# Optimization experiments

Measured on AMD Instinct MI355X. Metric: run time of the kernel, lower is better.

The kernel has to match this reference:

```python
import jax, jax.numpy as jnp
import numpy as np

IN_F = 1024
OUT_F = 1024
GRID_SIZE = 5
SPLINE_ORDER = 3
GRID_RANGE = (-1.0, 1.0)


def _make_grid():
    h = (GRID_RANGE[1] - GRID_RANGE[0]) / GRID_SIZE
    g = jnp.arange(-SPLINE_ORDER, GRID_SIZE + SPLINE_ORDER + 1, dtype=jnp.float32) * h + GRID_RANGE[0]
    return jnp.broadcast_to(g, (IN_F, g.shape[0]))  # (F, grid_size + 2*order + 1)


def setup_inputs() -> dict:
    key = jax.random.key(0)
    k1, k2, k3, k4 = jax.random.split(key, 4)
    B = 8192
    x = jax.random.normal(k1, (B, IN_F), dtype=jnp.float32)
    base_weight = jax.random.normal(k2, (OUT_F, IN_F), dtype=jnp.float32) / np.sqrt(IN_F)
    # mimic reset_parameters: uniform noise scaled by scale_noise/grid_size
    spline_weight = (jax.random.uniform(k3, (OUT_F, IN_F, GRID_SIZE + SPLINE_ORDER)) - 0.5) * (0.1 / GRID_SIZE)
    spline_scaler = jax.random.normal(k4, (OUT_F, IN_F), dtype=jnp.float32) / np.sqrt(IN_F)
    grid = _make_grid()
    return {"x": x, "base_weight": base_weight, "spline_weight": spline_weight,
            "spline_scaler": spline_scaler, "grid": grid}


def b_splines(x, grid):
    # x: (B, F); grid: (F, G) with G = grid_size + 2*order + 1
    xe = x[:, :, None]  # (B, F, 1)
    bases = ((xe >= grid[:, :-1]) & (xe < grid[:, 1:])).astype(x.dtype)  # (B, F, G-1)
    for k in range(1, SPLINE_ORDER + 1):
        left = (xe - grid[:, : -(k + 1)]) / (grid[:, k:-1] - grid[:, : -(k + 1)])
        right = (grid[:, k + 1 :] - xe) / (grid[:, k + 1 :] - grid[:, 1:-k])
        bases = left * bases[:, :, :-1] + right * bases[:, :, 1:]
    return bases  # (B, F, grid_size + order)


def reference(x, base_weight, spline_weight, spline_scaler, grid):
    base_out = jax.nn.silu(x) @ base_weight.T  # (B, O)
    basis = b_splines(x, grid)  # (B, F, C)
    scaled_w = spline_weight * spline_scaler[:, :, None]  # (O, F, C)
    spline_out = jnp.einsum('bfc,ofc->bo', basis, scaled_w)
    return base_out + spline_out
```

## Files before the change

### kernel.cpp

```cpp
#include <hip/hip_runtime.h>
#include <hip/hip_bf16.h>

#define IN_F   1024
#define OUT_F  1024
#define NCH    9
#define KDIM   (IN_F * NCH)
#define BATCH  8192

#define BM 256
#define BN 128
#define BK 64
#define NT (KDIM / BK)
#define ABUF_OFF (BM * BK)
#define BUFSZ (BM * BK + BN * BK)

typedef __attribute__((ext_vector_type(4))) float  f32x4;
typedef __attribute__((ext_vector_type(8))) __bf16 bf16x8;

typedef __attribute__((address_space(3))) unsigned short       lds_u16;
typedef const __attribute__((address_space(1))) unsigned short glb_u16;

__device__ inline unsigned short f2bf(float f) {
    union { float f; unsigned int u; } v; v.f = f;
    unsigned int u = v.u;
    unsigned int r = (u + 0x7FFFu + ((u >> 16) & 1u)) >> 16;
    return (unsigned short)r;
}

__global__ void wgt_kernel(const float* __restrict__ bw,
                           const float* __restrict__ sw,
                           const float* __restrict__ sc,
                           unsigned short* __restrict__ W) {
    int idx = blockIdx.x * blockDim.x + threadIdx.x;
    if (idx >= OUT_F * IN_F) return;
    float scale = sc[idx];
    const float4* swp = (const float4*)(sw + (size_t)idx * 8);
    float4 w0 = swp[0], w1 = swp[1];
    int o = idx >> 10, f = idx & 1023;
    size_t base = (size_t)o * KDIM + (size_t)f * NCH;
    W[base + 0] = f2bf(w0.x * scale);
    W[base + 1] = f2bf(w0.y * scale);
    W[base + 2] = f2bf(w0.z * scale);
    W[base + 3] = f2bf(w0.w * scale);
    W[base + 4] = f2bf(w1.x * scale);
    W[base + 5] = f2bf(w1.y * scale);
    W[base + 6] = f2bf(w1.z * scale);
    W[base + 7] = f2bf(w1.w * scale);
    W[base + 8] = f2bf(bw[idx]);
}

__global__ void act_kernel(const float* __restrict__ x,
                           unsigned short* __restrict__ A,
                           int row0, int nrows) {
    int idx = blockIdx.x * blockDim.x + threadIdx.x;
    if (idx >= nrows * IN_F) return;
    int r = idx >> 10;
    int f = idx & 1023;
    float xv = x[(size_t)(row0 + r) * IN_F + f];

    float s = xv / (1.0f + __expf(-xv));

    float t  = (xv + 2.2f) * 2.5f;
    float jf = floorf(t);
    int   j  = (int)jf;
    float u  = t - jf;
    float u2 = u * u, u3 = u2 * u;
    float p0 = u3 * (1.0f / 6.0f);
    float p1 = (-3.0f * u3 + 3.0f * u2 + 3.0f * u + 1.0f) * (1.0f / 6.0f);
    float p2 = (3.0f * u3 - 6.0f * u2 + 4.0f) * (1.0f / 6.0f);
    float om = 1.0f - u;
    float p3 = om * om * om * (1.0f / 6.0f);
    bool valid = (xv >= -2.2f) && (xv < 2.2f);

    unsigned short outv[NCH];
#pragma unroll
    for (int c = 0; c < 8; ++c) {
        int p = j - c;
        float v = 0.0f;
        if (valid)
            v = (p == 0) ? p0 : (p == 1) ? p1 : (p == 2) ? p2 : (p == 3) ? p3 : 0.0f;
        outv[c] = f2bf(v);
    }
    outv[8] = f2bf(s);

    size_t base = (size_t)r * KDIM + (size_t)f * NCH;
#pragma unroll
    for (int c = 0; c < NCH; ++c) A[base + c] = outv[c];
}


#define DECLA(i) \
    const int ciA##i = (i) * 512 + tid; \
    const unsigned short* srcA##i = A + (size_t)(m0 + (ciA##i >> 3)) * KDIM \
        + ((((ciA##i) & 7) ^ ((ciA##i >> 3) & 7)) << 3); \
    const int ldsA##i = (ciA##i) << 3;

#define DECLB(i) \
    const int ciB##i = (i) * 512 + tid; \
    const unsigned short* srcB##i = W + (size_t)(n0 + (ciB##i >> 3)) * KDIM \
        + ((((ciB##i) & 7) ^ ((ciB##i >> 3) & 7)) << 3); \
    const int ldsB##i = ABUF_OFF + ((ciB##i) << 3);

#define STAGE_A(i) do { \
    __builtin_amdgcn_global_load_lds((glb_u16*)srcA##i, (lds_u16*)nb + ldsA##i, 16, 0, 0); \
    srcA##i += BK; } while (0)

#define STAGE_B(i) do { \
    __builtin_amdgcn_global_load_lds((glb_u16*)srcB##i, (lds_u16*)nb + ldsB##i, 16, 0, 0); \
    srcB##i += BK; } while (0)

#define RDA(mi, kk) (*(const bf16x8*)&bufA[(rowa + (mi) * 16) * BK + ((((kk) * 4 + lhi) ^ l7) << 3)])
#define RDB(ni, kk) (*(const bf16x8*)&bufB[(rowb + (ni) * 16) * BK + ((((kk) * 4 + lhi) ^ l7) << 3)])

#define MM(mi, ni) do { \
    acc[mi][ni] = __builtin_amdgcn_mfma_f32_16x16x32_bf16(a##mi##0, b##ni##0, acc[mi][ni], 0, 0, 0); \
    acc[mi][ni] = __builtin_amdgcn_mfma_f32_16x16x32_bf16(a##mi##1, b##ni##1, acc[mi][ni], 0, 0, 0); \
} while (0)

__global__ __launch_bounds__(512, 2) void gemm_8p(
    const unsigned short* __restrict__ A,
    const unsigned short* __restrict__ W,
    float* __restrict__ C, int mblocks) {
    __shared__ unsigned short lds[2 * BUFSZ];

    const int tid  = threadIdx.x;
    const int wave = tid >> 6;
    const int lane = tid & 63;
    const int lm16 = lane & 15;
    const int lhi  = lane >> 4;
    const int l7   = lane & 7;

    const int l  = (blockIdx.x & 7) * mblocks + (blockIdx.x >> 3);
    const int lm = l >> 3;
    const int ln = l & 7;
    const int m0 = lm * BM;
    const int n0 = ln * BN;

    const int wr = wave >> 1;
    const int wc = wave & 1;
    const int rowa = wr * 64 + lm16;
    const int rowb = wc * 64 + lm16;

    f32x4 acc[4][4];
#pragma unroll
    for (int i = 0; i < 4; ++i)
#pragma unroll
        for (int jn = 0; jn < 4; ++jn) acc[i][jn] = (f32x4)(0.0f);

    DECLA(0) DECLA(1) DECLA(2) DECLA(3)
    DECLB(0) DECLB(1)

    {
        unsigned short* nb = lds;
        STAGE_A(0); STAGE_A(1); STAGE_A(2); STAGE_A(3);
        STAGE_B(0); STAGE_B(1);
        asm volatile("s_waitcnt vmcnt(0)" ::: "memory");
        __builtin_amdgcn_s_barrier();
    }

    for (int t = 0; t < NT; ++t) {
        const unsigned short* bufA = lds + (t & 1) * BUFSZ;
        const unsigned short* bufB = bufA + ABUF_OFF;
        unsigned short* nb = lds + ((t & 1) ^ 1) * BUFSZ;
        const bool pf = (t + 1 < NT);

        bf16x8 a00, a01, a10, a11, a20, a21, a30, a31;
        bf16x8 b00, b01, b10, b11, b20, b21, b30, b31;

        a00 = RDA(0, 0); a01 = RDA(0, 1); a10 = RDA(1, 0); a11 = RDA(1, 1);
        b00 = RDB(0, 0); b01 = RDB(0, 1); b10 = RDB(1, 0); b11 = RDB(1, 1);
        if (pf) { STAGE_A(0); STAGE_A(1); }
        __builtin_amdgcn_s_barrier();
        __builtin_amdgcn_s_setprio(1);
        MM(0, 0); MM(0, 1); MM(1, 0); MM(1, 1);
        __builtin_amdgcn_s_setprio(0);
        __builtin_amdgcn_s_barrier();

        b20 = RDB(2, 0); b21 = RDB(2, 1); b30 = RDB(3, 0); b31 = RDB(3, 1);
        if (pf) { STAGE_A(2); STAGE_A(3); }
        __builtin_amdgcn_s_barrier();
        __builtin_amdgcn_s_setprio(1);
        MM(0, 2); MM(0, 3); MM(1, 2); MM(1, 3);
        __builtin_amdgcn_s_setprio(0);
        __builtin_amdgcn_s_barrier();

        a20 = RDA(2, 0); a21 = RDA(2, 1); a30 = RDA(3, 0); a31 = RDA(3, 1);
        if (pf) { STAGE_B(0); STAGE_B(1); }
        __builtin_amdgcn_s_barrier();
        __builtin_amdgcn_s_setprio(1);
        MM(2, 2); MM(2, 3); MM(3, 2); MM(3, 3);
        __builtin_amdgcn_s_setprio(0);
        __builtin_amdgcn_s_barrier();

        __builtin_amdgcn_s_setprio(1);
        MM(2, 0); MM(2, 1); MM(3, 0); MM(3, 1);
        __builtin_amdgcn_s_setprio(0);
        asm volatile("s_waitcnt vmcnt(0)" ::: "memory");
        __builtin_amdgcn_s_barrier();
    }

    const int col0 = n0 + wc * 64 + lm16;
    const int row0 = m0 + wr * 64 + (lhi << 2);
#pragma unroll
    for (int mi = 0; mi < 4; ++mi)
#pragma unroll
        for (int ni = 0; ni < 4; ++ni)
#pragma unroll
            for (int r = 0; r < 4; ++r)
                C[(size_t)(row0 + mi * 16 + r) * OUT_F + (col0 + ni * 16)] = acc[mi][ni][r];
}

extern "C" void kernel_launch(void* const* d_in, const int* in_sizes, int n_in,
                              void* d_out, int out_size, void* d_ws, size_t ws_size,
                              hipStream_t stream) {
    const float* x             = (const float*)d_in[0];
    const float* base_weight   = (const float*)d_in[1];
    const float* spline_weight = (const float*)d_in[2];
    const float* spline_scaler = (const float*)d_in[3];
    float* out = (float*)d_out;

    unsigned short* Wc = (unsigned short*)d_ws;
    const size_t wbytes = (size_t)OUT_F * KDIM * sizeof(unsigned short);
    unsigned short* Abuf = (unsigned short*)((char*)d_ws + wbytes);

    size_t avail = ws_size > wbytes ? ws_size - wbytes : 0;
    long max_rows = (long)(avail / ((size_t)KDIM * sizeof(unsigned short)));
    int chunk = (max_rows >= BATCH) ? BATCH : (int)((max_rows / BM) * BM);
    if (chunk <= 0) chunk = BM;

    wgt_kernel<<<(OUT_F * IN_F + 255) / 256, 256, 0, stream>>>(
        base_weight, spline_weight, spline_scaler, Wc);

    for (int r0 = 0; r0 < BATCH; r0 += chunk) {
        int rows = (BATCH - r0) < chunk ? (BATCH - r0) : chunk;
        act_kernel<<<(rows * IN_F + 255) / 256, 256, 0, stream>>>(x, Abuf, r0, rows);
        int mblocks = rows / BM;
        gemm_8p<<<mblocks * 8, 512, 0, stream>>>(Abuf, Wc, out + (size_t)r0 * OUT_F, mblocks);
    }
}
```

Baseline: 216.4 us.

## Vectorize prep kernels, triple-buffer GEMM LDS, drop chunked launch loop

```diff
diff --git a/kernel.cpp b/kernel.cpp
--- a/kernel.cpp
+++ b/kernel.cpp
@@ -32,60 +32,88 @@
                            const float* __restrict__ sc,
                            unsigned short* __restrict__ W) {
     int idx = blockIdx.x * blockDim.x + threadIdx.x;
-    if (idx >= OUT_F * IN_F) return;
-    float scale = sc[idx];
-    const float4* swp = (const float4*)(sw + (size_t)idx * 8);
-    float4 w0 = swp[0], w1 = swp[1];
-    int o = idx >> 10, f = idx & 1023;
-    size_t base = (size_t)o * KDIM + (size_t)f * NCH;
-    W[base + 0] = f2bf(w0.x * scale);
-    W[base + 1] = f2bf(w0.y * scale);
-    W[base + 2] = f2bf(w0.z * scale);
-    W[base + 3] = f2bf(w0.w * scale);
-    W[base + 4] = f2bf(w1.x * scale);
-    W[base + 5] = f2bf(w1.y * scale);
-    W[base + 6] = f2bf(w1.z * scale);
-    W[base + 7] = f2bf(w1.w * scale);
-    W[base + 8] = f2bf(bw[idx]);
+    if (idx >= OUT_F * (IN_F / 8)) return;
+    const float4* swp = (const float4*)(sw + (size_t)idx * 64);
+    const float4* scp = (const float4*)(sc + (size_t)idx * 8);
+    const float4* bwp = (const float4*)(bw + (size_t)idx * 8);
+    float4 sc0 = scp[0], sc1 = scp[1];
+    float4 bw0 = bwp[0], bw1 = bwp[1];
+    float scl[8] = {sc0.x, sc0.y, sc0.z, sc0.w, sc1.x, sc1.y, sc1.z, sc1.w};
+    float bas[8] = {bw0.x, bw0.y, bw0.z, bw0.w, bw1.x, bw1.y, bw1.z, bw1.w};
+
+    unsigned short tmp[72];
+#pragma unroll
+    for (int e = 0; e < 8; ++e) {
+        float4 w0 = swp[e * 2], w1 = swp[e * 2 + 1];
+        float s = scl[e];
+        tmp[e * 9 + 0] = f2bf(w0.x * s);
+        tmp[e * 9 + 1] = f2bf(w0.y * s);
+        tmp[e * 9 + 2] = f2bf(w0.z * s);
+        tmp[e * 9 + 3] = f2bf(w0.w * s);
+        tmp[e * 9 + 4] = f2bf(w1.x * s);
+        tmp[e * 9 + 5] = f2bf(w1.y * s);
+        tmp[e * 9 + 6] = f2bf(w1.z * s);
+        tmp[e * 9 + 7] = f2bf(w1.w * s);
+        tmp[e * 9 + 8] = f2bf(bas[e]);
+    }
+    unsigned int u[36];
+#pragma unroll
+    for (int k = 0; k < 36; ++k)
+        u[k] = (unsigned int)tmp[2 * k] | ((unsigned int)tmp[2 * k + 1] << 16);
+    uint4* dst = (uint4*)(W + (size_t)idx * 72);
+#pragma unroll
+    for (int i = 0; i < 9; ++i) {
+        uint4 v; v.x = u[i * 4]; v.y = u[i * 4 + 1]; v.z = u[i * 4 + 2]; v.w = u[i * 4 + 3];
+        dst[i] = v;
+    }
 }
 
 __global__ void act_kernel(const float* __restrict__ x,
-                           unsigned short* __restrict__ A,
-                           int row0, int nrows) {
+                           unsigned short* __restrict__ A) {
     int idx = blockIdx.x * blockDim.x + threadIdx.x;
-    if (idx >= nrows * IN_F) return;
-    int r = idx >> 10;
-    int f = idx & 1023;
-    float xv = x[(size_t)(row0 + r) * IN_F + f];
-
-    float s = xv / (1.0f + __expf(-xv));
-
-    float t  = (xv + 2.2f) * 2.5f;
-    float jf = floorf(t);
-    int   j  = (int)jf;
-    float u  = t - jf;
-    float u2 = u * u, u3 = u2 * u;
-    float p0 = u3 * (1.0f / 6.0f);
-    float p1 = (-3.0f * u3 + 3.0f * u2 + 3.0f * u + 1.0f) * (1.0f / 6.0f);
-    float p2 = (3.0f * u3 - 6.0f * u2 + 4.0f) * (1.0f / 6.0f);
-    float om = 1.0f - u;
-    float p3 = om * om * om * (1.0f / 6.0f);
-    bool valid = (xv >= -2.2f) && (xv < 2.2f);
-
-    unsigned short outv[NCH];
-#pragma unroll
-    for (int c = 0; c < 8; ++c) {
-        int p = j - c;
-        float v = 0.0f;
-        if (valid)
-            v = (p == 0) ? p0 : (p == 1) ? p1 : (p == 2) ? p2 : (p == 3) ? p3 : 0.0f;
-        outv[c] = f2bf(v);
-    }
-    outv[8] = f2bf(s);
-
-    size_t base = (size_t)r * KDIM + (size_t)f * NCH;
-#pragma unroll
-    for (int c = 0; c < NCH; ++c) A[base + c] = outv[c];
+    if (idx >= BATCH * (IN_F / 8)) return;
+    const float4* xp = (const float4*)(x + (size_t)idx * 8);
+    float4 x0 = xp[0], x1 = xp[1];
+    float xs[8] = {x0.x, x0.y, x0.z, x0.w, x1.x, x1.y, x1.z, x1.w};
+
+    unsigned short tmp[72];
+#pragma unroll
+    for (int e = 0; e < 8; ++e) {
+        float xv = xs[e];
+        float s  = xv / (1.0f + __expf(-xv));
+
+        float t  = (xv + 2.2f) * 2.5f;
+        float jf = floorf(t);
+        int   j  = (int)jf;
+        float u  = t - jf;
+        float u2 = u * u, u3 = u2 * u;
+        float p0 = u3 * (1.0f / 6.0f);
+        float p1 = (-3.0f * u3 + 3.0f * u2 + 3.0f * u + 1.0f) * (1.0f / 6.0f);
+        float p2 = (3.0f * u3 - 6.0f * u2 + 4.0f) * (1.0f / 6.0f);
+        float om = 1.0f - u;
+        float p3 = om * om * om * (1.0f / 6.0f);
+        bool valid = (xv >= -2.2f) && (xv < 2.2f);
+
+#pragma unroll
+        for (int c = 0; c < 8; ++c) {
+            int p = j - c;
+            float v = 0.0f;
+            if (valid)
+                v = (p == 0) ? p0 : (p == 1) ? p1 : (p == 2) ? p2 : (p == 3) ? p3 : 0.0f;
+            tmp[e * 9 + c] = f2bf(v);
+        }
+        tmp[e * 9 + 8] = f2bf(s);
+    }
+    unsigned int u[36];
+#pragma unroll
+    for (int k = 0; k < 36; ++k)
+        u[k] = (unsigned int)tmp[2 * k] | ((unsigned int)tmp[2 * k + 1] << 16);
+    uint4* dst = (uint4*)(A + (size_t)idx * 72);
+#pragma unroll
+    for (int i = 0; i < 9; ++i) {
+        uint4 v; v.x = u[i * 4]; v.y = u[i * 4 + 1]; v.z = u[i * 4 + 2]; v.w = u[i * 4 + 3];
+        dst[i] = v;
+    }
 }
 
 
@@ -117,11 +145,11 @@
     acc[mi][ni] = __builtin_amdgcn_mfma_f32_16x16x32_bf16(a##mi##1, b##ni##1, acc[mi][ni], 0, 0, 0); \
 } while (0)
 
-__global__ __launch_bounds__(512, 2) void gemm_8p(
+__global__ __launch_bounds__(512, 2) void gemm_3b(
     const unsigned short* __restrict__ A,
     const unsigned short* __restrict__ W,
     float* __restrict__ C, int mblocks) {
-    __shared__ unsigned short lds[2 * BUFSZ];
+    __shared__ unsigned short lds[3 * BUFSZ];
 
     const int tid  = threadIdx.x;
     const int wave = tid >> 6;
@@ -152,17 +180,21 @@
 
     {
         unsigned short* nb = lds;
-        STAGE_A(0); STAGE_A(1); STAGE_A(2); STAGE_A(3);
-        STAGE_B(0); STAGE_B(1);
-        asm volatile("s_waitcnt vmcnt(0)" ::: "memory");
-        __builtin_amdgcn_s_barrier();
-    }
-
+        STAGE_A(0); STAGE_A(1); STAGE_A(2); STAGE_A(3); STAGE_B(0); STAGE_B(1);
+    }
+    {
+        unsigned short* nb = lds + BUFSZ;
+        STAGE_A(0); STAGE_A(1); STAGE_A(2); STAGE_A(3); STAGE_B(0); STAGE_B(1);
+    }
+    asm volatile("s_waitcnt vmcnt(6)" ::: "memory");
+    __builtin_amdgcn_s_barrier();
+
+    int cb = 0;
     for (int t = 0; t < NT; ++t) {
-        const unsigned short* bufA = lds + (t & 1) * BUFSZ;
+        const unsigned short* bufA = lds + cb * BUFSZ;
         const unsigned short* bufB = bufA + ABUF_OFF;
-        unsigned short* nb = lds + ((t & 1) ^ 1) * BUFSZ;
-        const bool pf = (t + 1 < NT);
+        unsigned short* nb = lds + (cb == 0 ? 2 * BUFSZ : (size_t)(cb - 1) * BUFSZ);
+        const bool pf = (t + 2 < NT);
 
         bf16x8 a00, a01, a10, a11, a20, a21, a30, a31;
         bf16x8 b00, b01, b10, b11, b20, b21, b30, b31;
@@ -195,8 +227,11 @@
         __builtin_amdgcn_s_setprio(1);
         MM(2, 0); MM(2, 1); MM(3, 0); MM(3, 1);
         __builtin_amdgcn_s_setprio(0);
-        asm volatile("s_waitcnt vmcnt(0)" ::: "memory");
-        __builtin_amdgcn_s_barrier();
+        if (pf) asm volatile("s_waitcnt vmcnt(6)" ::: "memory");
+        else    asm volatile("s_waitcnt vmcnt(0)" ::: "memory");
+        __builtin_amdgcn_s_barrier();
+
+        cb = (cb == 2) ? 0 : cb + 1;
     }
 
     const int col0 = n0 + wc * 64 + lm16;
@@ -223,18 +258,11 @@
     const size_t wbytes = (size_t)OUT_F * KDIM * sizeof(unsigned short);
     unsigned short* Abuf = (unsigned short*)((char*)d_ws + wbytes);
 
-    size_t avail = ws_size > wbytes ? ws_size - wbytes : 0;
-    long max_rows = (long)(avail / ((size_t)KDIM * sizeof(unsigned short)));
-    int chunk = (max_rows >= BATCH) ? BATCH : (int)((max_rows / BM) * BM);
-    if (chunk <= 0) chunk = BM;
-
-    wgt_kernel<<<(OUT_F * IN_F + 255) / 256, 256, 0, stream>>>(
+    wgt_kernel<<<(OUT_F * (IN_F / 8) + 255) / 256, 256, 0, stream>>>(
         base_weight, spline_weight, spline_scaler, Wc);
 
-    for (int r0 = 0; r0 < BATCH; r0 += chunk) {
-        int rows = (BATCH - r0) < chunk ? (BATCH - r0) : chunk;
-        act_kernel<<<(rows * IN_F + 255) / 256, 256, 0, stream>>>(x, Abuf, r0, rows);
-        int mblocks = rows / BM;
-        gemm_8p<<<mblocks * 8, 512, 0, stream>>>(Abuf, Wc, out + (size_t)r0 * OUT_F, mblocks);
-    }
-}
+    act_kernel<<<(BATCH * (IN_F / 8) + 255) / 256, 256, 0, stream>>>(x, Abuf);
+
+    int mblocks = BATCH / BM;
+    gemm_3b<<<mblocks * 8, 512, 0, stream>>>(Abuf, Wc, out, mblocks);
+}
```

Result: slower. 231.4 us (+6.9%).
